# Performance work log

Measured on AMD Instinct MI355X. Metric: run time of the kernel, lower is better.

Reference implementation:

```python
import jax, jax.numpy as jnp
import numpy as np

EMB = 512
HEADS = 8


def setup_inputs() -> dict:
    key = jax.random.key(0)
    ks = jax.random.split(key, 5)
    B, N, E = 4, 2048, EMB
    x = jax.random.normal(ks[0], (B, N, E), dtype=jnp.float32)
    # Linear weights stored [in, out] so y = x @ W + b (matches torch x @ W.T + b with W.T)
    W_qkv = jax.random.normal(ks[1], (E, 3 * E), dtype=jnp.float32) * (E ** -0.5)
    b_qkv = jax.random.normal(ks[2], (3 * E,), dtype=jnp.float32) * 0.02
    W_proj = jax.random.normal(ks[3], (E, E), dtype=jnp.float32) * (E ** -0.5)
    b_proj = jax.random.normal(ks[4], (E,), dtype=jnp.float32) * 0.02
    return {"x": x, "W_qkv": W_qkv, "b_qkv": b_qkv, "W_proj": W_proj, "b_proj": b_proj}


def reference(x, W_qkv, b_qkv, W_proj, b_proj):
    B, N, E = x.shape
    H = HEADS
    D = E // H
    qkv = x @ W_qkv + b_qkv                      # [B, N, 3E]
    # einops 'b n (h d qkv) -> qkv b h n d': last dim splits as (h, d, 3) -> q/k/v interleaved
    qkv = qkv.reshape(B, N, H, D, 3)
    q = jnp.transpose(qkv[..., 0], (0, 2, 1, 3))  # [B, H, N, D]
    k = jnp.transpose(qkv[..., 1], (0, 2, 1, 3))
    v = jnp.transpose(qkv[..., 2], (0, 2, 1, 3))
    scale = jnp.asarray(E, x.dtype) ** 0.5        # divides by sqrt(emb_size), as in source
    energies = jnp.einsum('bhqd,bhkd->bhqk', q, k) / scale
    attention = jax.nn.softmax(energies, axis=-1)
    out = jnp.einsum('bhqk,bhkd->bhqd', attention, v)
    out = jnp.transpose(out, (0, 2, 1, 3)).reshape(B, N, E)
    return out @ W_proj + b_proj
```

## Files before the change

### kernel.cpp

```cpp
#include <hip/hip_runtime.h>
#include <hip/hip_bf16.h>

typedef __hip_bfloat16 bf16;
typedef __attribute__((ext_vector_type(8))) short short8;
typedef __attribute__((ext_vector_type(4))) float f32x4;
typedef __attribute__((ext_vector_type(16))) float f32x16;

static constexpr float QSCALE = 1.4426950408889634f / 22.627416997969522f;

__device__ __forceinline__ void gload_lds16(const void* g, void* l) {
  __builtin_amdgcn_global_load_lds((const __attribute__((address_space(1))) unsigned*)(g),
                                   (__attribute__((address_space(3))) unsigned*)(l), 16, 0, 0);
}

__device__ __forceinline__ unsigned cvtpk(float a, float b) {
  unsigned r;
  asm("v_cvt_pk_bf16_f32 %0, %1, %2" : "=v"(r) : "v"(a), "v"(b));
  return r;
}

__device__ __forceinline__ void packP(const f32x16& s, short8* pb) {
#pragma unroll
  for (int g = 0; g < 2; ++g) {
    unsigned a0 = cvtpk(s[8 * g + 0], s[8 * g + 1]);
    unsigned a1 = cvtpk(s[8 * g + 2], s[8 * g + 3]);
    unsigned b0 = cvtpk(s[8 * g + 4], s[8 * g + 5]);
    unsigned b1 = cvtpk(s[8 * g + 6], s[8 * g + 7]);
    asm("v_permlane32_swap_b32 %0, %1" : "+v"(a0), "+v"(b0));
    asm("v_permlane32_swap_b32 %0, %1" : "+v"(a1), "+v"(b1));
    union { unsigned u[4]; short8 v; } pu;
    pu.u[0] = a0; pu.u[1] = a1; pu.u[2] = b0; pu.u[3] = b1;
    pb[g] = pu.v;
  }
}

__global__ __launch_bounds__(256) void prep_kernel(const float* __restrict__ x,
                                                   bf16* __restrict__ xb,
                                                   const float* __restrict__ Wqkv,
                                                   bf16* __restrict__ Wqkvt,
                                                   const float* __restrict__ Wproj,
                                                   bf16* __restrict__ Wprojt) {
  __shared__ float tile[64][65];
  const int bid = blockIdx.x;
  if (bid < 2048) {
    const int i = bid * 256 + threadIdx.x;
    const float4* src = (const float4*)(x) + (size_t)i * 2;
    float4 a = src[0], b = src[1];
    union { short8 v; unsigned u[4]; } o;
    o.u[0] = cvtpk(a.x, a.y);
    o.u[1] = cvtpk(a.z, a.w);
    o.u[2] = cvtpk(b.x, b.y);
    o.u[3] = cvtpk(b.z, b.w);
    *(short8*)(xb + (size_t)i * 8) = o.v;
  } else {
    const float* W;
    bf16* Wt;
    int Nout, permute, j0, k0;
    if (bid < 2048 + 192) {
      const int tb = bid - 2048;
      W = Wqkv; Wt = Wqkvt; Nout = 1536; permute = 1;
      j0 = (tb % 24) * 64; k0 = (tb / 24) * 64;
    } else {
      const int tb = bid - 2240;
      W = Wproj; Wt = Wprojt; Nout = 512; permute = 0;
      j0 = (tb % 8) * 64; k0 = (tb / 8) * 64;
    }
    const int tx = threadIdx.x & 63, ty = threadIdx.x >> 6;
    for (int r = ty; r < 64; r += 4)
      tile[r][tx] = W[(size_t)(k0 + r) * Nout + j0 + tx];
    __syncthreads();
    for (int r = ty; r < 64; r += 4) {
      int j = j0 + r;
      int jp = j;
      if (permute) {
        int h = j / 192, rr = j % 192, d = rr / 3, s = rr % 3;
        jp = s * 512 + h * 64 + d;
      }
      Wt[(size_t)jp * 512 + k0 + tx] = __float2bfloat16(tile[tx][r]);
    }
  }
}

__global__ __launch_bounds__(256, 3) void gemm_qkv(const bf16* __restrict__ A,
                                                   const bf16* __restrict__ Bt,
                                                   const float* __restrict__ bias,
                                                   bf16* __restrict__ Qb,
                                                   bf16* __restrict__ Kb,
                                                   bf16* __restrict__ Vt) {
  __shared__ short Alds[128 * 64];
  __shared__ short Blds[128 * 64];
  const int t = threadIdx.x;
  const int w = t >> 6;
  const int wr = w >> 1, wc = w & 1;
  const int lr = t & 15;
  const int lq = (t >> 4) & 3;
  const int bid = blockIdx.x;
  const int jj = bid >> 3;
  const int bm = (bid & 7) + 8 * (jj / 12);
  const int bn = jj % 12;

  f32x4 acc[4][4];
#pragma unroll
  for (int m = 0; m < 4; ++m)
#pragma unroll
    for (int n = 0; n < 4; ++n)
#pragma unroll
      for (int j = 0; j < 4; ++j) acc[m][n][j] = 0.f;

  for (int kt = 0; kt < 8; ++kt) {
#pragma unroll
    for (int i = 0; i < 4; ++i) {
      const int c = i * 256 + t, r = c >> 3, g = (c & 7) ^ (r & 7);
      gload_lds16(A + (size_t)(bm * 128 + r) * 512 + kt * 64 + g * 8,
                  &Alds[(i * 256 + w * 64) * 8]);
    }
#pragma unroll
    for (int i = 0; i < 4; ++i) {
      const int c = i * 256 + t, r = c >> 3, g = (c & 7) ^ (r & 7);
      gload_lds16(Bt + (size_t)(bn * 128 + r) * 512 + kt * 64 + g * 8,
                  &Blds[(i * 256 + w * 64) * 8]);
    }
    __syncthreads();
#pragma unroll
    for (int kh2 = 0; kh2 < 2; ++kh2) {
      short8 af[4], bfr[4];
#pragma unroll
      for (int m = 0; m < 4; ++m)
        af[m] = *(const short8*)&Alds[(wr * 64 + m * 16 + lr) * 64 +
                                      ((((kh2 << 2) | lq) ^ (lr & 7)) << 3)];
#pragma unroll
      for (int n = 0; n < 4; ++n)
        bfr[n] = *(const short8*)&Blds[(wc * 64 + n * 16 + lr) * 64 +
                                       ((((kh2 << 2) | lq) ^ (lr & 7)) << 3)];
#pragma unroll
      for (int m = 0; m < 4; ++m)
#pragma unroll
        for (int n = 0; n < 4; ++n)
          acc[m][n] = __builtin_amdgcn_mfma_f32_16x16x32_bf16(af[m], bfr[n], acc[m][n], 0, 0, 0);
    }
    __syncthreads();
  }

#pragma unroll
  for (int m = 0; m < 4; ++m) {
#pragma unroll
    for (int n = 0; n < 4; ++n) {
      const int col = bn * 128 + wc * 64 + n * 16 + lr;
      const int s = col >> 9, h = (col >> 6) & 7, d = col & 63;
      const float bv = bias[h * 192 + d * 3 + s];
      const int hd = col & 511;
#pragma unroll
      for (int j = 0; j < 4; ++j) {
        const int row = bm * 128 + wr * 64 + m * 16 + lq * 4 + j;
        const float v = acc[m][n][j] + bv;
        if (s == 0)
          Qb[(size_t)row * 512 + hd] = __float2bfloat16(v * QSCALE);
        else if (s == 1)
          Kb[(size_t)row * 512 + hd] = __float2bfloat16(v);
        else
          Vt[((size_t)((row >> 11) * 8 + h) * 64 + d) * 2048 + (row & 2047)] =
              __float2bfloat16(v);
      }
    }
  }
}

__global__ __launch_bounds__(256, 2) void gemm_proj(const bf16* __restrict__ A,
                                                    const bf16* __restrict__ Bt,
                                                    const float* __restrict__ bias,
                                                    float* __restrict__ Cout) {
  __shared__ short Alds[128 * 64];
  __shared__ short Blds[64 * 64];
  const int t = threadIdx.x;
  const int w = t >> 6;
  const int wr = w >> 1, wc = w & 1;
  const int lr = t & 15;
  const int lq = (t >> 4) & 3;
  const int bid = blockIdx.x;
  const int jj = bid >> 3;
  const int bm = (bid & 7) + 8 * (jj >> 3);
  const int bn = jj & 7;

  f32x4 acc[4][2];
#pragma unroll
  for (int m = 0; m < 4; ++m)
#pragma unroll
    for (int n = 0; n < 2; ++n)
#pragma unroll
      for (int j = 0; j < 4; ++j) acc[m][n][j] = 0.f;

  for (int kt = 0; kt < 8; ++kt) {
#pragma unroll
    for (int i = 0; i < 4; ++i) {
      const int c = i * 256 + t, r = c >> 3, g = (c & 7) ^ (r & 7);
      gload_lds16(A + (size_t)(bm * 128 + r) * 512 + kt * 64 + g * 8,
                  &Alds[(i * 256 + w * 64) * 8]);
    }
#pragma unroll
    for (int i = 0; i < 2; ++i) {
      const int c = i * 256 + t, r = c >> 3, g = (c & 7) ^ (r & 7);
      gload_lds16(Bt + (size_t)(bn * 64 + r) * 512 + kt * 64 + g * 8,
                  &Blds[(i * 256 + w * 64) * 8]);
    }
    __syncthreads();
#pragma unroll
    for (int kh2 = 0; kh2 < 2; ++kh2) {
      short8 af[4], bfr[2];
#pragma unroll
      for (int m = 0; m < 4; ++m)
        af[m] = *(const short8*)&Alds[(wr * 64 + m * 16 + lr) * 64 +
                                      ((((kh2 << 2) | lq) ^ (lr & 7)) << 3)];
#pragma unroll
      for (int n = 0; n < 2; ++n)
        bfr[n] = *(const short8*)&Blds[(wc * 32 + n * 16 + lr) * 64 +
                                       ((((kh2 << 2) | lq) ^ (lr & 7)) << 3)];
#pragma unroll
      for (int m = 0; m < 4; ++m)
#pragma unroll
        for (int n = 0; n < 2; ++n)
          acc[m][n] = __builtin_amdgcn_mfma_f32_16x16x32_bf16(af[m], bfr[n], acc[m][n], 0, 0, 0);
    }
    __syncthreads();
  }

#pragma unroll
  for (int m = 0; m < 4; ++m) {
#pragma unroll
    for (int n = 0; n < 2; ++n) {
      const int col = bn * 64 + wc * 32 + n * 16 + lr;
      const float bv = bias[col];
#pragma unroll
      for (int j = 0; j < 4; ++j) {
        const int row = bm * 128 + wr * 64 + m * 16 + lq * 4 + j;
        Cout[(size_t)row * 512 + col] = acc[m][n][j] + bv;
      }
    }
  }
}

__global__ __launch_bounds__(256, 2) void attn_fwd(const bf16* __restrict__ Q,
                                                   const bf16* __restrict__ K,
                                                   const bf16* __restrict__ Vt,
                                                   bf16* __restrict__ O) {
  __shared__ short Klds[2][128 * 64];
  __shared__ short Vlds[2][64 * 128];
  __shared__ float dnm[2][128];
  const int t = threadIdx.x;
  const int w = t >> 6;
  const int qw = w & 1;
  const int kh = w >> 1;
  const int l = t & 63;
  const int lo = l & 31;
  const int hi = l >> 5;
  const int bid = blockIdx.x;
  const int bh = bid & 31, qt = bid >> 5;
  const int b = bh >> 3, h = bh & 7;
  const int qgA = qt * 128 + qw * 64 + lo;

  const bf16* Kb = K + (size_t)b * 2048 * 512 + h * 64;
  const bf16* Vb = Vt + (size_t)bh * 64 * 2048;

  const bf16* qptrA = Q + ((size_t)b * 2048 + qgA) * 512 + h * 64 + hi * 8;
  short8 qfA[4], qfB[4];
#pragma unroll
  for (int kk = 0; kk < 4; ++kk) {
    qfA[kk] = *(const short8*)(qptrA + kk * 16);
    qfB[kk] = *(const short8*)(qptrA + 32 * 512 + kk * 16);
  }

  union { unsigned u[4]; short8 v; } ones;
#pragma unroll
  for (int j = 0; j < 4; ++j) ones.u[j] = 0x3F803F80u;

  f32x16 zv;
#pragma unroll
  for (int r = 0; r < 16; ++r) zv[r] = 0.f;

  f32x16 accA0, accA1, accB0, accB1;
  f32x16 ssumA, ssumB;
#pragma unroll
  for (int r = 0; r < 16; ++r) {
    accA0[r] = 0.f; accA1[r] = 0.f; accB0[r] = 0.f; accB1[r] = 0.f;
    ssumA[r] = 0.f; ssumB[r] = 0.f;
  }

#define STAGE(BUF, KV0)                                                              \
  do {                                                                               \
    _Pragma("unroll") for (int i = 0; i < 4; ++i) {                                  \
      const int c = i * 256 + t, r = c >> 3, g = (c & 7) ^ (r & 7);                  \
      gload_lds16(Kb + (size_t)((KV0) + r) * 512 + g * 8,                            \
                  &Klds[BUF][(i * 256 + w * 64) * 8]);                               \
    }                                                                                \
    _Pragma("unroll") for (int i = 0; i < 4; ++i) {                                  \
      const int c = i * 256 + t, r = c >> 4, g = (c & 15) ^ (r & 15);                \
      gload_lds16(Vb + (size_t)r * 2048 + (KV0) + g * 8,                             \
                  &Vlds[BUF][(i * 256 + w * 64) * 8]);                               \
    }                                                                                \
  } while (0)

  STAGE(0, 0);
  __syncthreads();

#pragma unroll 2
  for (int it = 0; it < 16; ++it) {
    const int buf = it & 1;
    if (it + 1 < 16) STAGE(buf ^ 1, (it + 1) * 128);

    const char* kl = (const char*)&Klds[buf][0];
    const char* vl = (const char*)&Vlds[buf][0];

#pragma unroll
    for (int sh = 0; sh < 2; ++sh) {
      short8 kf[4];
#pragma unroll
      for (int kk = 0; kk < 4; ++kk)
        kf[kk] = *(const short8*)(kl + ((kh * 64 + sh * 32 + lo) << 7) +
                                  ((((kk << 1) | hi) ^ (lo & 7)) << 4));

      f32x16 sA, sB;
      __builtin_amdgcn_s_setprio(1);
#pragma unroll
      for (int kk = 0; kk < 4; ++kk) {
        sA = __builtin_amdgcn_mfma_f32_32x32x16_bf16(kf[kk], qfA[kk], kk ? sA : zv, 0, 0, 0);
        sB = __builtin_amdgcn_mfma_f32_32x32x16_bf16(kf[kk], qfB[kk], kk ? sB : zv, 0, 0, 0);
      }
      __builtin_amdgcn_s_setprio(0);

      short8 vf[2][2];
#pragma unroll
      for (int dt = 0; dt < 2; ++dt)
#pragma unroll
        for (int j = 0; j < 2; ++j)
          vf[dt][j] = *(const short8*)(vl + ((dt * 32 + lo) << 8) +
                                       ((((kh << 3) | (sh << 2) | (j << 1) | hi) ^ (lo & 15))
                                        << 4));

#pragma unroll
      for (int r = 0; r < 16; ++r) sA[r] = __builtin_amdgcn_exp2f(sA[r]);
#pragma unroll
      for (int r = 0; r < 16; ++r) sB[r] = __builtin_amdgcn_exp2f(sB[r]);
      short8 pbA[2], pbB[2];
      packP(sA, pbA);
      packP(sB, pbB);

      __builtin_amdgcn_s_setprio(1);
#pragma unroll
      for (int j = 0; j < 2; ++j) {
        accA0 = __builtin_amdgcn_mfma_f32_32x32x16_bf16(vf[0][j], pbA[j], accA0, 0, 0, 0);
        accA1 = __builtin_amdgcn_mfma_f32_32x32x16_bf16(vf[1][j], pbA[j], accA1, 0, 0, 0);
        accB0 = __builtin_amdgcn_mfma_f32_32x32x16_bf16(vf[0][j], pbB[j], accB0, 0, 0, 0);
        accB1 = __builtin_amdgcn_mfma_f32_32x32x16_bf16(vf[1][j], pbB[j], accB1, 0, 0, 0);
        ssumA = __builtin_amdgcn_mfma_f32_32x32x16_bf16(ones.v, pbA[j], ssumA, 0, 0, 0);
        ssumB = __builtin_amdgcn_mfma_f32_32x32x16_bf16(ones.v, pbB[j], ssumB, 0, 0, 0);
      }
      __builtin_amdgcn_s_setprio(0);
    }

    __syncthreads();
  }
#undef STAGE

  float lsA = ssumA[0], lsB = ssumB[0];
  float* base = qw ? (float*)&Vlds[0][0] : (float*)&Klds[0][0];
  if (kh) {
#pragma unroll
    for (int r = 0; r < 16; ++r) {
      base[l * 64 + ((r + l) & 63)] = accA0[r];
      base[l * 64 + ((16 + r + l) & 63)] = accA1[r];
      base[l * 64 + ((32 + r + l) & 63)] = accB0[r];
      base[l * 64 + ((48 + r + l) & 63)] = accB1[r];
    }
    dnm[qw][l] = lsA;
    dnm[qw][64 + l] = lsB;
  }
  __syncthreads();
  if (!kh) {
#pragma unroll
    for (int r = 0; r < 16; ++r) {
      accA0[r] += base[l * 64 + ((r + l) & 63)];
      accA1[r] += base[l * 64 + ((16 + r + l) & 63)];
      accB0[r] += base[l * 64 + ((32 + r + l) & 63)];
      accB1[r] += base[l * 64 + ((48 + r + l) & 63)];
    }
    lsA += dnm[qw][l];
    lsB += dnm[qw][64 + l];
    const float rlA = 1.0f / lsA;
    const float rlB = 1.0f / lsB;
    bf16* opA = O + ((size_t)b * 2048 + qgA) * 512 + h * 64;
    bf16* opB = opA + 32 * 512;
#pragma unroll
    for (int r = 0; r < 16; ++r) {
      const int d = (r & 3) + 8 * (r >> 2) + 4 * hi;
      opA[d] = __float2bfloat16(accA0[r] * rlA);
      opA[32 + d] = __float2bfloat16(accA1[r] * rlA);
      opB[d] = __float2bfloat16(accB0[r] * rlB);
      opB[32 + d] = __float2bfloat16(accB1[r] * rlB);
    }
  }
}

extern "C" void kernel_launch(void* const* d_in, const int* in_sizes, int n_in,
                              void* d_out, int out_size, void* d_ws, size_t ws_size,
                              hipStream_t stream) {
  const float* x = (const float*)d_in[0];
  const float* Wqkv = (const float*)d_in[1];
  const float* bqkv = (const float*)d_in[2];
  const float* Wproj = (const float*)d_in[3];
  const float* bproj = (const float*)d_in[4];
  float* out = (float*)d_out;

  char* ws = (char*)d_ws;
  bf16* xb = (bf16*)ws;
  bf16* Wqkvt = xb + (size_t)8192 * 512;
  bf16* Wprojt = Wqkvt + (size_t)1536 * 512;
  bf16* Qb = Wprojt + (size_t)512 * 512;
  bf16* Kb = Qb + (size_t)8192 * 512;
  bf16* Vt = Kb + (size_t)8192 * 512;
  bf16* Ob = xb;

  prep_kernel<<<2304, 256, 0, stream>>>(x, xb, Wqkv, Wqkvt, Wproj, Wprojt);
  gemm_qkv<<<768, 256, 0, stream>>>(xb, Wqkvt, bqkv, Qb, Kb, Vt);
  attn_fwd<<<512, 256, 0, stream>>>(Qb, Kb, Vt, Ob);
  gemm_proj<<<512, 256, 0, stream>>>(Ob, Wprojt, bproj, out);
}
```

Measured before the change: 94.31 us.

## Fuse x fp32-to-bf16 conversion into QKV GEMM and restructure attention inner loop

The separate pass that converted x to bf16 is removed. The QKV GEMM now loads fp32 x directly, converts it in registers and writes bf16 into LDS, which avoids writing and re-reading an 8 MB intermediate. In exchange the A tile is loaded synchronously through registers instead of the async global_load_lds path, and each block re-reads and re-converts the same x rows across its 12 column tiles. The attention inner loop is also manually split so both halves' QK^T MFMAs are issued back to back, which raises register pressure.

```diff
diff --git a/kernel.cpp b/kernel.cpp
--- a/kernel.cpp
+++ b/kernel.cpp
@@ -34,54 +34,39 @@
   }
 }
 
-__global__ __launch_bounds__(256) void prep_kernel(const float* __restrict__ x,
-                                                   bf16* __restrict__ xb,
-                                                   const float* __restrict__ Wqkv,
-                                                   bf16* __restrict__ Wqkvt,
-                                                   const float* __restrict__ Wproj,
-                                                   bf16* __restrict__ Wprojt) {
+__global__ __launch_bounds__(256) void prep_w(const float* __restrict__ Wqkv,
+                                              bf16* __restrict__ Wqkvt,
+                                              const float* __restrict__ Wproj,
+                                              bf16* __restrict__ Wprojt) {
   __shared__ float tile[64][65];
   const int bid = blockIdx.x;
-  if (bid < 2048) {
-    const int i = bid * 256 + threadIdx.x;
-    const float4* src = (const float4*)(x) + (size_t)i * 2;
-    float4 a = src[0], b = src[1];
-    union { short8 v; unsigned u[4]; } o;
-    o.u[0] = cvtpk(a.x, a.y);
-    o.u[1] = cvtpk(a.z, a.w);
-    o.u[2] = cvtpk(b.x, b.y);
-    o.u[3] = cvtpk(b.z, b.w);
-    *(short8*)(xb + (size_t)i * 8) = o.v;
+  const float* W;
+  bf16* Wt;
+  int Nout, permute, j0, k0;
+  if (bid < 192) {
+    W = Wqkv; Wt = Wqkvt; Nout = 1536; permute = 1;
+    j0 = (bid % 24) * 64; k0 = (bid / 24) * 64;
   } else {
-    const float* W;
-    bf16* Wt;
-    int Nout, permute, j0, k0;
-    if (bid < 2048 + 192) {
-      const int tb = bid - 2048;
-      W = Wqkv; Wt = Wqkvt; Nout = 1536; permute = 1;
-      j0 = (tb % 24) * 64; k0 = (tb / 24) * 64;
-    } else {
-      const int tb = bid - 2240;
-      W = Wproj; Wt = Wprojt; Nout = 512; permute = 0;
-      j0 = (tb % 8) * 64; k0 = (tb / 8) * 64;
-    }
-    const int tx = threadIdx.x & 63, ty = threadIdx.x >> 6;
-    for (int r = ty; r < 64; r += 4)
-      tile[r][tx] = W[(size_t)(k0 + r) * Nout + j0 + tx];
-    __syncthreads();
-    for (int r = ty; r < 64; r += 4) {
-      int j = j0 + r;
-      int jp = j;
-      if (permute) {
-        int h = j / 192, rr = j % 192, d = rr / 3, s = rr % 3;
-        jp = s * 512 + h * 64 + d;
-      }
-      Wt[(size_t)jp * 512 + k0 + tx] = __float2bfloat16(tile[tx][r]);
-    }
-  }
-}
-
-__global__ __launch_bounds__(256, 3) void gemm_qkv(const bf16* __restrict__ A,
+    const int tb = bid - 192;
+    W = Wproj; Wt = Wprojt; Nout = 512; permute = 0;
+    j0 = (tb % 8) * 64; k0 = (tb / 8) * 64;
+  }
+  const int tx = threadIdx.x & 63, ty = threadIdx.x >> 6;
+  for (int r = ty; r < 64; r += 4)
+    tile[r][tx] = W[(size_t)(k0 + r) * Nout + j0 + tx];
+  __syncthreads();
+  for (int r = ty; r < 64; r += 4) {
+    int j = j0 + r;
+    int jp = j;
+    if (permute) {
+      int h = j / 192, rr = j % 192, d = rr / 3, s = rr % 3;
+      jp = s * 512 + h * 64 + d;
+    }
+    Wt[(size_t)jp * 512 + k0 + tx] = __float2bfloat16(tile[tx][r]);
+  }
+}
+
+__global__ __launch_bounds__(256, 3) void gemm_qkv(const float* __restrict__ X,
                                                    const bf16* __restrict__ Bt,
                                                    const float* __restrict__ bias,
                                                    bf16* __restrict__ Qb,
@@ -110,9 +95,16 @@
   for (int kt = 0; kt < 8; ++kt) {
 #pragma unroll
     for (int i = 0; i < 4; ++i) {
-      const int c = i * 256 + t, r = c >> 3, g = (c & 7) ^ (r & 7);
-      gload_lds16(A + (size_t)(bm * 128 + r) * 512 + kt * 64 + g * 8,
-                  &Alds[(i * 256 + w * 64) * 8]);
+      const int c = i * 256 + t, r = c >> 3, cc = c & 7, g = cc ^ (r & 7);
+      const float* src = X + (size_t)(bm * 128 + r) * 512 + kt * 64 + cc * 8;
+      const float4 a = *(const float4*)src;
+      const float4 b2 = *(const float4*)(src + 4);
+      union { short8 v; unsigned u[4]; } o;
+      o.u[0] = cvtpk(a.x, a.y);
+      o.u[1] = cvtpk(a.z, a.w);
+      o.u[2] = cvtpk(b2.x, b2.y);
+      o.u[3] = cvtpk(b2.z, b2.w);
+      *(short8*)&Alds[r * 64 + g * 8] = o.v;
     }
 #pragma unroll
     for (int i = 0; i < 4; ++i) {
@@ -309,52 +301,81 @@
     const char* kl = (const char*)&Klds[buf][0];
     const char* vl = (const char*)&Vlds[buf][0];
 
-#pragma unroll
-    for (int sh = 0; sh < 2; ++sh) {
-      short8 kf[4];
-#pragma unroll
-      for (int kk = 0; kk < 4; ++kk)
-        kf[kk] = *(const short8*)(kl + ((kh * 64 + sh * 32 + lo) << 7) +
-                                  ((((kk << 1) | hi) ^ (lo & 7)) << 4));
-
-      f32x16 sA, sB;
-      __builtin_amdgcn_s_setprio(1);
-#pragma unroll
-      for (int kk = 0; kk < 4; ++kk) {
-        sA = __builtin_amdgcn_mfma_f32_32x32x16_bf16(kf[kk], qfA[kk], kk ? sA : zv, 0, 0, 0);
-        sB = __builtin_amdgcn_mfma_f32_32x32x16_bf16(kf[kk], qfB[kk], kk ? sB : zv, 0, 0, 0);
-      }
-      __builtin_amdgcn_s_setprio(0);
-
-      short8 vf[2][2];
-#pragma unroll
-      for (int dt = 0; dt < 2; ++dt)
-#pragma unroll
-        for (int j = 0; j < 2; ++j)
-          vf[dt][j] = *(const short8*)(vl + ((dt * 32 + lo) << 8) +
-                                       ((((kh << 3) | (sh << 2) | (j << 1) | hi) ^ (lo & 15))
-                                        << 4));
-
-#pragma unroll
-      for (int r = 0; r < 16; ++r) sA[r] = __builtin_amdgcn_exp2f(sA[r]);
-#pragma unroll
-      for (int r = 0; r < 16; ++r) sB[r] = __builtin_amdgcn_exp2f(sB[r]);
-      short8 pbA[2], pbB[2];
-      packP(sA, pbA);
-      packP(sB, pbB);
-
-      __builtin_amdgcn_s_setprio(1);
-#pragma unroll
-      for (int j = 0; j < 2; ++j) {
-        accA0 = __builtin_amdgcn_mfma_f32_32x32x16_bf16(vf[0][j], pbA[j], accA0, 0, 0, 0);
-        accA1 = __builtin_amdgcn_mfma_f32_32x32x16_bf16(vf[1][j], pbA[j], accA1, 0, 0, 0);
-        accB0 = __builtin_amdgcn_mfma_f32_32x32x16_bf16(vf[0][j], pbB[j], accB0, 0, 0, 0);
-        accB1 = __builtin_amdgcn_mfma_f32_32x32x16_bf16(vf[1][j], pbB[j], accB1, 0, 0, 0);
-        ssumA = __builtin_amdgcn_mfma_f32_32x32x16_bf16(ones.v, pbA[j], ssumA, 0, 0, 0);
-        ssumB = __builtin_amdgcn_mfma_f32_32x32x16_bf16(ones.v, pbB[j], ssumB, 0, 0, 0);
-      }
-      __builtin_amdgcn_s_setprio(0);
-    }
+    short8 kf0[4], kf1[4];
+#pragma unroll
+    for (int kk = 0; kk < 4; ++kk) {
+      const int coff = (((kk << 1) | hi) ^ (lo & 7)) << 4;
+      kf0[kk] = *(const short8*)(kl + ((kh * 64 + lo) << 7) + coff);
+      kf1[kk] = *(const short8*)(kl + ((kh * 64 + 32 + lo) << 7) + coff);
+    }
+
+    f32x16 sA0, sB0, sA1, sB1;
+    __builtin_amdgcn_s_setprio(1);
+#pragma unroll
+    for (int kk = 0; kk < 4; ++kk) {
+      sA0 = __builtin_amdgcn_mfma_f32_32x32x16_bf16(kf0[kk], qfA[kk], kk ? sA0 : zv, 0, 0, 0);
+      sB0 = __builtin_amdgcn_mfma_f32_32x32x16_bf16(kf0[kk], qfB[kk], kk ? sB0 : zv, 0, 0, 0);
+    }
+#pragma unroll
+    for (int kk = 0; kk < 4; ++kk) {
+      sA1 = __builtin_amdgcn_mfma_f32_32x32x16_bf16(kf1[kk], qfA[kk], kk ? sA1 : zv, 0, 0, 0);
+      sB1 = __builtin_amdgcn_mfma_f32_32x32x16_bf16(kf1[kk], qfB[kk], kk ? sB1 : zv, 0, 0, 0);
+    }
+    __builtin_amdgcn_s_setprio(0);
+
+    short8 vf0[2][2];
+#pragma unroll
+    for (int dt = 0; dt < 2; ++dt)
+#pragma unroll
+      for (int j = 0; j < 2; ++j)
+        vf0[dt][j] = *(const short8*)(vl + ((dt * 32 + lo) << 8) +
+                                      ((((kh << 3) | (j << 1) | hi) ^ (lo & 15)) << 4));
+#pragma unroll
+    for (int r = 0; r < 16; ++r) sA0[r] = __builtin_amdgcn_exp2f(sA0[r]);
+#pragma unroll
+    for (int r = 0; r < 16; ++r) sB0[r] = __builtin_amdgcn_exp2f(sB0[r]);
+    short8 pbA0[2], pbB0[2];
+    packP(sA0, pbA0);
+    packP(sB0, pbB0);
+
+    __builtin_amdgcn_s_setprio(1);
+#pragma unroll
+    for (int j = 0; j < 2; ++j) {
+      accA0 = __builtin_amdgcn_mfma_f32_32x32x16_bf16(vf0[0][j], pbA0[j], accA0, 0, 0, 0);
+      accA1 = __builtin_amdgcn_mfma_f32_32x32x16_bf16(vf0[1][j], pbA0[j], accA1, 0, 0, 0);
+      accB0 = __builtin_amdgcn_mfma_f32_32x32x16_bf16(vf0[0][j], pbB0[j], accB0, 0, 0, 0);
+      accB1 = __builtin_amdgcn_mfma_f32_32x32x16_bf16(vf0[1][j], pbB0[j], accB1, 0, 0, 0);
+      ssumA = __builtin_amdgcn_mfma_f32_32x32x16_bf16(ones.v, pbA0[j], ssumA, 0, 0, 0);
+      ssumB = __builtin_amdgcn_mfma_f32_32x32x16_bf16(ones.v, pbB0[j], ssumB, 0, 0, 0);
+    }
+    __builtin_amdgcn_s_setprio(0);
+
+    short8 vf1[2][2];
+#pragma unroll
+    for (int dt = 0; dt < 2; ++dt)
+#pragma unroll
+      for (int j = 0; j < 2; ++j)
+        vf1[dt][j] = *(const short8*)(vl + ((dt * 32 + lo) << 8) +
+                                      ((((kh << 3) | 4 | (j << 1) | hi) ^ (lo & 15)) << 4));
+#pragma unroll
+    for (int r = 0; r < 16; ++r) sA1[r] = __builtin_amdgcn_exp2f(sA1[r]);
+#pragma unroll
+    for (int r = 0; r < 16; ++r) sB1[r] = __builtin_amdgcn_exp2f(sB1[r]);
+    short8 pbA1[2], pbB1[2];
+    packP(sA1, pbA1);
+    packP(sB1, pbB1);
+
+    __builtin_amdgcn_s_setprio(1);
+#pragma unroll
+    for (int j = 0; j < 2; ++j) {
+      accA0 = __builtin_amdgcn_mfma_f32_32x32x16_bf16(vf1[0][j], pbA1[j], accA0, 0, 0, 0);
+      accA1 = __builtin_amdgcn_mfma_f32_32x32x16_bf16(vf1[1][j], pbA1[j], accA1, 0, 0, 0);
+      accB0 = __builtin_amdgcn_mfma_f32_32x32x16_bf16(vf1[0][j], pbB1[j], accB0, 0, 0, 0);
+      accB1 = __builtin_amdgcn_mfma_f32_32x32x16_bf16(vf1[1][j], pbB1[j], accB1, 0, 0, 0);
+      ssumA = __builtin_amdgcn_mfma_f32_32x32x16_bf16(ones.v, pbA1[j], ssumA, 0, 0, 0);
+      ssumB = __builtin_amdgcn_mfma_f32_32x32x16_bf16(ones.v, pbB1[j], ssumB, 0, 0, 0);
+    }
+    __builtin_amdgcn_s_setprio(0);
 
     __syncthreads();
   }
@@ -410,16 +431,15 @@
   float* out = (float*)d_out;
 
   char* ws = (char*)d_ws;
-  bf16* xb = (bf16*)ws;
-  bf16* Wqkvt = xb + (size_t)8192 * 512;
+  bf16* Ob = (bf16*)ws;
+  bf16* Wqkvt = Ob + (size_t)8192 * 512;
   bf16* Wprojt = Wqkvt + (size_t)1536 * 512;
   bf16* Qb = Wprojt + (size_t)512 * 512;
   bf16* Kb = Qb + (size_t)8192 * 512;
   bf16* Vt = Kb + (size_t)8192 * 512;
-  bf16* Ob = xb;
-
-  prep_kernel<<<2304, 256, 0, stream>>>(x, xb, Wqkv, Wqkvt, Wproj, Wprojt);
-  gemm_qkv<<<768, 256, 0, stream>>>(xb, Wqkvt, bqkv, Qb, Kb, Vt);
+
+  prep_w<<<256, 256, 0, stream>>>(Wqkv, Wqkvt, Wproj, Wprojt);
+  gemm_qkv<<<768, 256, 0, stream>>>(x, Wqkvt, bqkv, Qb, Kb, Vt);
   attn_fwd<<<512, 256, 0, stream>>>(Qb, Kb, Vt, Ob);
   gemm_proj<<<512, 256, 0, stream>>>(Ob, Wprojt, bproj, out);
 }
```

Measured after the change: 103.7 us. 10.0% more time.
